# Kernel tuning notes

Measured on AMD Instinct MI355X. Metric: run time of the kernel, lower is better.

## Reference

```python
import jax, jax.numpy as jnp
import numpy as np

N, D, H, L = 50000, 128, 4, 3
E = 800000
C = D // H            # head dim = 32
NEG_SLOPE = 0.2       # PyG GATv2Conv default negative_slope
LN_EPS = 1e-5         # nn.LayerNorm default eps


def setup_inputs() -> dict:
    key = jax.random.key(0)
    ks = jax.random.split(key, 8)
    s = 1.0 / np.sqrt(D).astype(np.float32)
    return {
        "fine_poi_x": jax.random.normal(ks[0], (N, D), jnp.float32),
        "edge_index": jax.random.randint(ks[1], (2, E), 0, N, dtype=jnp.int32),
        "Wl": jax.random.normal(ks[2], (L, D, D), jnp.float32) * s,
        "bl": jnp.zeros((L, D), jnp.float32),
        "Wr": jax.random.normal(ks[3], (L, D, D), jnp.float32) * s,
        "br": jnp.zeros((L, D), jnp.float32),
        "att": jax.random.normal(ks[4], (L, H, C), jnp.float32) * s,
        "bias": jnp.zeros((L, D), jnp.float32),
        "gamma": jnp.ones((L, D), jnp.float32),
        "beta": jnp.zeros((L, D), jnp.float32),
    }


def _gatv2_conv(x, src, dst, Wl, bl, Wr, br, att, bias):
    # x: [N, D]; src/dst: [E'] (self-loops already appended)
    xl = (x @ Wl + bl).reshape(N, H, C)   # source-side transform (lin_l)
    xr = (x @ Wr + br).reshape(N, H, C)   # target-side transform (lin_r)
    m = xl[src] + xr[dst]                 # [E', H, C] per-edge pre-activation
    m = jax.nn.leaky_relu(m, NEG_SLOPE)
    e = jnp.einsum("ehc,hc->eh", m, att)  # [E', H] attention logits
    # segment softmax over edges grouped by destination node
    emax = jax.ops.segment_max(e, dst, num_segments=N)      # [N, H]
    ee = jnp.exp(e - emax[dst])
    denom = jax.ops.segment_sum(ee, dst, num_segments=N)    # [N, H]
    alpha = ee / denom[dst]               # self-loops guarantee denom >= 1 term
    out = jax.ops.segment_sum(xl[src] * alpha[:, :, None], dst, num_segments=N)
    return out.reshape(N, D) + bias


def _layernorm(x, g, b):
    mu = jnp.mean(x, axis=-1, keepdims=True)
    var = jnp.var(x, axis=-1, keepdims=True)
    return (x - mu) * jax.lax.rsqrt(var + LN_EPS) * g + b


def reference(fine_poi_x, edge_index, Wl, bl, Wr, br, att, bias, gamma, beta):
    # PyG GATv2Conv add_self_loops=True: append i->i edges
    loops = jnp.arange(N, dtype=edge_index.dtype)
    src = jnp.concatenate([edge_index[0], loops])
    dst = jnp.concatenate([edge_index[1], loops])
    x = fine_poi_x
    for i in range(L):
        h = _gatv2_conv(x, src, dst, Wl[i], bl[i], Wr[i], br[i], att[i], bias[i])
        x = _layernorm(x + h, gamma[i], beta[i])
        if i != L - 1:
            x = jax.nn.relu(x)
    return x
```

## Files before the change

kernel.cpp:

```cpp
#include <hip/hip_runtime.h>

#define N_NODES 50000
#define N_EDGES 800000
#define DIM 128
#define TOT_EDGES (N_EDGES + N_NODES)
#define LOG2E 1.44269504088896f

#define BSHIFT 9
#define BNODES 512
#define NB ((N_NODES + BNODES - 1) / BNODES)
#define BCAP 16384
#define EPB 4096
#define EPT 16
#define NBLK_A ((TOT_EDGES + EPB - 1) / EPB)

typedef __attribute__((ext_vector_type(8))) _Float16 f16x8;
typedef __attribute__((ext_vector_type(2))) _Float16 h2;
typedef __attribute__((ext_vector_type(4))) float f32x4;
typedef decltype(__builtin_amdgcn_cvt_pkrtz(0.f, 0.f)) fp16v2;

__device__ inline uint h2u(h2 v) { return __builtin_bit_cast(uint, v); }
__device__ inline h2 u2h(uint v) { return __builtin_bit_cast(h2, v); }
__device__ inline uint pk2u(fp16v2 v) { return __builtin_bit_cast(uint, v); }

__device__ inline float rowsum16(float v) {
  int x;
  x = __builtin_amdgcn_update_dpp(0, __float_as_int(v), 0x128, 0xF, 0xF, true);
  v += __int_as_float(x);
  x = __builtin_amdgcn_update_dpp(0, __float_as_int(v), 0x124, 0xF, 0xF, true);
  v += __int_as_float(x);
  x = __builtin_amdgcn_update_dpp(0, __float_as_int(v), 0x122, 0xF, 0xF, true);
  v += __int_as_float(x);
  x = __builtin_amdgcn_update_dpp(0, __float_as_int(v), 0x121, 0xF, 0xF, true);
  v += __int_as_float(x);
  return v;
}

__device__ inline float quadsum4(float v) {
  int x;
  x = __builtin_amdgcn_update_dpp(0, __float_as_int(v), 0xB1, 0xF, 0xF, true);
  v += __int_as_float(x);
  x = __builtin_amdgcn_update_dpp(0, __float_as_int(v), 0x4E, 0xF, 0xF, true);
  v += __int_as_float(x);
  return v;
}


__global__ __launch_bounds__(256) void partA_kernel(const int* __restrict__ srcArr,
                                                    const int* __restrict__ dstArr,
                                                    int* __restrict__ bcnt,
                                                    uint2* __restrict__ bbuf) {
  int tid = threadIdx.x;
  int e0 = blockIdx.x * EPB;
  __shared__ int hist[NB], base[NB], loff[NB];
  if (tid < NB) { hist[tid] = 0; loff[tid] = 0; }
  __syncthreads();

  int sv[EPT], dv[EPT];
#pragma unroll
  for (int i = 0; i < EPT; ++i) {
    int e = e0 + i * 256 + tid;
    int s = 0, d = -1;
    if (e < TOT_EDGES) {
      if (e < N_EDGES) { s = srcArr[e]; d = dstArr[e]; }
      else { s = e - N_EDGES; d = s; }
    }
    sv[i] = s; dv[i] = d;
    if (d >= 0) atomicAdd(&hist[d >> BSHIFT], 1);
  }
  __syncthreads();
  if (tid < NB) {
    int h = hist[tid];
    if (h > 0) base[tid] = atomicAdd(&bcnt[tid], h);
  }
  __syncthreads();
#pragma unroll
  for (int i = 0; i < EPT; ++i) {
    int d = dv[i];
    if (d >= 0) {
      int b = d >> BSHIFT;
      int p = atomicAdd(&loff[b], 1);
      bbuf[(size_t)b * BCAP + base[b] + p] = make_uint2((uint)sv[i], (uint)d);
    }
  }
}

__global__ __launch_bounds__(128) void scanb_kernel(const int* __restrict__ bcnt,
                                                    int* __restrict__ colbase,
                                                    int* __restrict__ rowptr) {
  int tid = threadIdx.x;
  int v = (tid < NB) ? bcnt[tid] : 0;
  __shared__ int s[128];
  s[tid] = v;
  __syncthreads();
  for (int off = 1; off < 128; off <<= 1) {
    int t = (tid >= off) ? s[tid - off] : 0;
    __syncthreads();
    s[tid] += t;
    __syncthreads();
  }
  if (tid < NB) colbase[tid] = s[tid] - v;
  if (tid == 0) rowptr[N_NODES] = TOT_EDGES;
}

__global__ __launch_bounds__(512) void partB_kernel(const uint2* __restrict__ bbuf,
                                                    const int* __restrict__ bcnt,
                                                    const int* __restrict__ colbase,
                                                    int* __restrict__ rowptr,
                                                    int* __restrict__ col) {
  int b = blockIdx.x, tid = threadIdx.x;
  int m = bcnt[b];
  int cb = colbase[b];
  const uint2* buf = bbuf + (size_t)b * BCAP;

  __shared__ int cnt[BNODES], scn[BNODES], cur[BNODES];
  cnt[tid] = 0;
  __syncthreads();
  for (int e = tid; e < m; e += 512) {
    int d = (int)buf[e].y;
    atomicAdd(&cnt[d & (BNODES - 1)], 1);
  }
  __syncthreads();
  int c = cnt[tid];
  scn[tid] = c;
  __syncthreads();
  for (int off = 1; off < BNODES; off <<= 1) {
    int t = (tid >= off) ? scn[tid - off] : 0;
    __syncthreads();
    scn[tid] += t;
    __syncthreads();
  }
  int excl = scn[tid] - c;
  int node = b * BNODES + tid;
  if (node < N_NODES) rowptr[node] = cb + excl;
  cur[tid] = excl;
  __syncthreads();
  for (int e = tid; e < m; e += 512) {
    uint2 sd = buf[e];
    int p = atomicAdd(&cur[(int)sd.y & (BNODES - 1)], 1);
    col[cb + p] = (int)sd.x;
  }
}


__global__ __launch_bounds__(256) void convx_kernel(const float* __restrict__ x,
                                                    uint* __restrict__ xb) {
  int t = blockIdx.x * 256 + threadIdx.x;
  if (t < N_NODES * (DIM / 2)) {
    float2 v = ((const float2*)x)[t];
    xb[t] = pk2u(__builtin_amdgcn_cvt_pkrtz(v.x, v.y));
  }
}

__global__ __launch_bounds__(256) void convw_kernel(const float* __restrict__ Wl,
                                                    const float* __restrict__ Wr,
                                                    ushort* __restrict__ Wt) {
  int t = blockIdx.x * 256 + threadIdx.x;
  if (t >= 3 * 2 * DIM * DIM) return;
  int k = t & 127;
  int n = (t >> 7) & 127;
  int w = (t >> 14) & 1;
  int l = t >> 15;
  const float* W = w ? Wr : Wl;
  _Float16 h = (_Float16)W[l * DIM * DIM + k * DIM + n];
  Wt[t] = __builtin_bit_cast(ushort, h);
}

__global__ __launch_bounds__(192) void conva_kernel(const float* __restrict__ att,
                                                    uint* __restrict__ attc) {
  int t = threadIdx.x;
  float a0 = att[2 * t] * LOG2E, a1 = att[2 * t + 1] * LOG2E;
  attc[t] = pk2u(__builtin_amdgcn_cvt_pkrtz(a0, a1));
}


__global__ __launch_bounds__(256) void gemm_mfma_kernel(
    const uint* __restrict__ xb,
    const ushort* __restrict__ Wt,
    const float* __restrict__ bl, const float* __restrict__ br,
    uint* __restrict__ xl, uint* __restrict__ xr) {
  int wave = threadIdx.x >> 6, lane = threadIdx.x & 63;
  int lr = lane & 15, kq = lane >> 4;
  int m0 = blockIdx.x * 64;

  const ushort* W = Wt + (wave >> 1) * (DIM * DIM);
  const float* bias = (wave >> 1) ? br : bl;
  uint* outp = (wave >> 1) ? xr : xl;
  int n0 = (wave & 1) * 64;

  f16x8 bfrag[4][4];
#pragma unroll
  for (int nt = 0; nt < 4; ++nt)
#pragma unroll
    for (int kt = 0; kt < 4; ++kt)
      bfrag[nt][kt] = *(const f16x8*)(W + (n0 + nt * 16 + lr) * DIM + kt * 32 + kq * 8);

  f32x4 acc[4][4];
#pragma unroll
  for (int mt = 0; mt < 4; ++mt)
#pragma unroll
    for (int nt = 0; nt < 4; ++nt)
      acc[mt][nt] = (f32x4){0.f, 0.f, 0.f, 0.f};

#pragma unroll
  for (int mt = 0; mt < 4; ++mt) {
    int m = m0 + mt * 16 + lr;
    int mc = m < N_NODES ? m : N_NODES - 1;
    f16x8 afrag[4];
#pragma unroll
    for (int kt = 0; kt < 4; ++kt)
      afrag[kt] = *(const f16x8*)((const ushort*)xb + (size_t)mc * DIM + kt * 32 + kq * 8);
#pragma unroll
    for (int nt = 0; nt < 4; ++nt)
#pragma unroll
      for (int kt = 0; kt < 4; ++kt)
        acc[mt][nt] = __builtin_amdgcn_mfma_f32_16x16x32_f16(bfrag[nt][kt], afrag[kt],
                                                             acc[mt][nt], 0, 0, 0);
  }

#pragma unroll
  for (int mt = 0; mt < 4; ++mt) {
    int m = m0 + mt * 16 + lr;
    if (m < N_NODES) {
#pragma unroll
      for (int nt = 0; nt < 4; ++nt) {
        int n = n0 + nt * 16 + kq * 4;
        float4 bb = *(const float4*)(bias + n);
        uint2 o;
        o.x = pk2u(__builtin_amdgcn_cvt_pkrtz(acc[mt][nt][0] + bb.x, acc[mt][nt][1] + bb.y));
        o.y = pk2u(__builtin_amdgcn_cvt_pkrtz(acc[mt][nt][2] + bb.z, acc[mt][nt][3] + bb.w));
        *(uint2*)(outp + (size_t)m * (DIM / 2) + (n >> 1)) = o;
      }
    }
  }
}


__global__ __launch_bounds__(64) void att_kernel(
    const uint4* __restrict__ xinb, const uint4* __restrict__ xlb,
    const uint4* __restrict__ xrb, const int* __restrict__ rowptr,
    const int* __restrict__ col, const uint4* __restrict__ attc,
    const float4* __restrict__ bias, const float4* __restrict__ gamma,
    const float4* __restrict__ beta, uint4* __restrict__ xoutb,
    float4* __restrict__ xoutf, int do_relu) {
  int lane = threadIdx.x;
  int j = lane & 15, e4 = lane >> 4;
  int n = blockIdx.x;

  uint4 rq = xrb[n * 16 + j];
  uint4 aq = attc[j];
  h2 r2[4] = {u2h(rq.x), u2h(rq.y), u2h(rq.z), u2h(rq.w)};
  h2 at2[4] = {u2h(aq.x), u2h(aq.y), u2h(aq.z), u2h(aq.w)};
  const h2 c02 = {(_Float16)0.2f, (_Float16)0.2f};

  h2 accp[4] = {};
  float den = 0.f;

  int js = rowptr[n], je = rowptr[n + 1];
  int jm = je - 1;

  int ci;
  ci = js + e4;      int cA = col[ci < jm ? ci : jm];
  ci = js + 4 + e4;  int cB = col[ci < jm ? ci : jm];
  ci = js + 8 + e4;  int cC = col[ci < jm ? ci : jm];
  uint4 gA = xlb[(size_t)cA * 16 + j];
  uint4 gB = xlb[(size_t)cB * 16 + j];

  for (int cbase = js; cbase < je; cbase += 4) {
    ci = cbase + 12 + e4;
    int cD = col[ci < jm ? ci : jm];
    uint4 gC = xlb[(size_t)cC * 16 + j];

    h2 a0 = u2h(gA.x), a1 = u2h(gA.y), a2 = u2h(gA.z), a3 = u2h(gA.w);
    float p = 0.f;
    {
      h2 s0 = a0 + r2[0], s1 = a1 + r2[1], s2 = a2 + r2[2], s3 = a3 + r2[3];
      h2 m0 = __builtin_elementwise_max(s0, s0 * c02);
      h2 m1 = __builtin_elementwise_max(s1, s1 * c02);
      h2 m2 = __builtin_elementwise_max(s2, s2 * c02);
      h2 m3 = __builtin_elementwise_max(s3, s3 * c02);
      p = __builtin_amdgcn_fdot2(__builtin_bit_cast(fp16v2, m0),
                                 __builtin_bit_cast(fp16v2, at2[0]), p, false);
      p = __builtin_amdgcn_fdot2(__builtin_bit_cast(fp16v2, m1),
                                 __builtin_bit_cast(fp16v2, at2[1]), p, false);
      p = __builtin_amdgcn_fdot2(__builtin_bit_cast(fp16v2, m2),
                                 __builtin_bit_cast(fp16v2, at2[2]), p, false);
      p = __builtin_amdgcn_fdot2(__builtin_bit_cast(fp16v2, m3),
                                 __builtin_bit_cast(fp16v2, at2[3]), p, false);
    }
    p = quadsum4(p);
    float w = (cbase + e4 < je) ? __builtin_amdgcn_exp2f(p) : 0.f;
    den += w;
    _Float16 wh = (_Float16)w;
    h2 w2 = {wh, wh};
    accp[0] = w2 * a0 + accp[0];
    accp[1] = w2 * a1 + accp[1];
    accp[2] = w2 * a2 + accp[2];
    accp[3] = w2 * a3 + accp[3];

    gA = gB; gB = gC; cC = cD;
  }

#pragma unroll
  for (int t = 0; t < 4; ++t) {
    accp[t] += u2h((uint)__shfl_xor((int)h2u(accp[t]), 16, 64));
    accp[t] += u2h((uint)__shfl_xor((int)h2u(accp[t]), 32, 64));
  }
  den += __shfl_xor(den, 16, 64);
  den += __shfl_xor(den, 32, 64);

  float inv = 1.0f / den;
  float acc[8];
#pragma unroll
  for (int t = 0; t < 4; ++t) {
    acc[2 * t] = (float)accp[t].x;
    acc[2 * t + 1] = (float)accp[t].y;
  }

  uint4 xi4 = xinb[n * 16 + j];
  h2 xi[4] = {u2h(xi4.x), u2h(xi4.y), u2h(xi4.z), u2h(xi4.w)};
  float4 b0 = bias[2 * j], b1 = bias[2 * j + 1];

  float o[8];
  o[0] = fmaf(acc[0], inv, b0.x + (float)xi[0].x);
  o[1] = fmaf(acc[1], inv, b0.y + (float)xi[0].y);
  o[2] = fmaf(acc[2], inv, b0.z + (float)xi[1].x);
  o[3] = fmaf(acc[3], inv, b0.w + (float)xi[1].y);
  o[4] = fmaf(acc[4], inv, b1.x + (float)xi[2].x);
  o[5] = fmaf(acc[5], inv, b1.y + (float)xi[2].y);
  o[6] = fmaf(acc[6], inv, b1.z + (float)xi[3].x);
  o[7] = fmaf(acc[7], inv, b1.w + (float)xi[3].y);

  float s1 = 0.f, s2 = 0.f;
#pragma unroll
  for (int t = 0; t < 8; ++t) { s1 += o[t]; s2 = fmaf(o[t], o[t], s2); }
  s1 = rowsum16(s1);
  s2 = rowsum16(s2);
  float mean = s1 * (1.0f / DIM);
  float var = s2 * (1.0f / DIM) - mean * mean;
  float rstd = rsqrtf(var + 1e-5f);

  float4 g0 = gamma[2 * j], g1 = gamma[2 * j + 1];
  float4 t0 = beta[2 * j], t1 = beta[2 * j + 1];
  float y[8];
  y[0] = (o[0] - mean) * rstd * g0.x + t0.x;
  y[1] = (o[1] - mean) * rstd * g0.y + t0.y;
  y[2] = (o[2] - mean) * rstd * g0.z + t0.z;
  y[3] = (o[3] - mean) * rstd * g0.w + t0.w;
  y[4] = (o[4] - mean) * rstd * g1.x + t1.x;
  y[5] = (o[5] - mean) * rstd * g1.y + t1.y;
  y[6] = (o[6] - mean) * rstd * g1.z + t1.z;
  y[7] = (o[7] - mean) * rstd * g1.w + t1.w;
  if (do_relu) {
#pragma unroll
    for (int t = 0; t < 8; ++t) y[t] = fmaxf(y[t], 0.f);
  }

  if (e4 == 0) {
    if (xoutb) {
      uint4 ov;
      ov.x = pk2u(__builtin_amdgcn_cvt_pkrtz(y[0], y[1]));
      ov.y = pk2u(__builtin_amdgcn_cvt_pkrtz(y[2], y[3]));
      ov.z = pk2u(__builtin_amdgcn_cvt_pkrtz(y[4], y[5]));
      ov.w = pk2u(__builtin_amdgcn_cvt_pkrtz(y[6], y[7]));
      xoutb[n * 16 + j] = ov;
    }
    if (xoutf) {
      xoutf[n * 32 + 2 * j] = make_float4(y[0], y[1], y[2], y[3]);
      xoutf[n * 32 + 2 * j + 1] = make_float4(y[4], y[5], y[6], y[7]);
    }
  }
}


extern "C" void kernel_launch(void* const* d_in, const int* in_sizes, int n_in,
                              void* d_out, int out_size, void* d_ws, size_t ws_size,
                              hipStream_t stream) {
  const float* x_in  = (const float*)d_in[0];
  const int*   eidx  = (const int*)d_in[1];
  const float* Wl    = (const float*)d_in[2];
  const float* bl    = (const float*)d_in[3];
  const float* Wr    = (const float*)d_in[4];
  const float* br    = (const float*)d_in[5];
  const float* att   = (const float*)d_in[6];
  const float* bias  = (const float*)d_in[7];
  const float* gamma = (const float*)d_in[8];
  const float* beta  = (const float*)d_in[9];
  float* out = (float*)d_out;

  char* p = (char*)d_ws;
  auto alloc = [&](size_t bytes) {
    char* q = p;
    p += (bytes + 255) & ~(size_t)255;
    return q;
  };
  uint*  xb       = (uint*)alloc((size_t)N_NODES * (DIM / 2) * 4);
  uint*  xlb      = (uint*)alloc((size_t)N_NODES * (DIM / 2) * 4);
  uint*  xrb      = (uint*)alloc((size_t)N_NODES * (DIM / 2) * 4);
  ushort* Wt      = (ushort*)alloc((size_t)3 * 2 * DIM * DIM * 2);
  uint*  attc     = (uint*)alloc((size_t)3 * 64 * 4);
  int*   rowptr   = (int*)alloc((size_t)(N_NODES + 1) * 4);
  int*   col      = (int*)alloc((size_t)TOT_EDGES * 4);
  uint2* bbuf     = (uint2*)alloc((size_t)NB * BCAP * 8);
  int*   bcnt     = (int*)alloc((size_t)NB * 4);
  int*   colbase  = (int*)alloc((size_t)NB * 4);

  (void)hipMemsetAsync(bcnt, 0, (size_t)NB * 4, stream);
  partA_kernel<<<NBLK_A, 256, 0, stream>>>(eidx, eidx + N_EDGES, bcnt, bbuf);
  scanb_kernel<<<1, 128, 0, stream>>>(bcnt, colbase, rowptr);
  partB_kernel<<<NB, 512, 0, stream>>>(bbuf, bcnt, colbase, rowptr, col);
  convx_kernel<<<(N_NODES * (DIM / 2) + 255) / 256, 256, 0, stream>>>(x_in, xb);
  convw_kernel<<<(3 * 2 * DIM * DIM + 255) / 256, 256, 0, stream>>>(Wl, Wr, Wt);
  conva_kernel<<<1, 192, 0, stream>>>(att, attc);

  for (int l = 0; l < 3; ++l) {
    gemm_mfma_kernel<<<(N_NODES + 63) / 64, 256, 0, stream>>>(
        xb, Wt + (size_t)l * 2 * DIM * DIM, bl + l * DIM, br + l * DIM, xlb, xrb);
    att_kernel<<<N_NODES, 64, 0, stream>>>(
        (const uint4*)xb, (const uint4*)xlb, (const uint4*)xrb, rowptr, col,
        (const uint4*)(attc + l * 64), (const float4*)(bias + l * DIM),
        (const float4*)(gamma + l * DIM), (const float4*)(beta + l * DIM),
        (l == 2) ? nullptr : (uint4*)xb, (l == 2) ? (float4*)out : nullptr,
        (l != 2) ? 1 : 0);
  }
}
```

Before: 248.8 us.

## Make attention kernel persistent with grid-stride waves and deeper gather prefetch

```diff
diff --git a/kernel.cpp b/kernel.cpp
--- a/kernel.cpp
+++ b/kernel.cpp
@@ -13,6 +13,9 @@
 #define EPB 4096
 #define EPT 16
 #define NBLK_A ((TOT_EDGES + EPB - 1) / EPB)
+
+#define ATT_BLOCKS 2048
+#define ATT_WAVES (ATT_BLOCKS * 4)
 
 typedef __attribute__((ext_vector_type(8))) _Float16 f16x8;
 typedef __attribute__((ext_vector_type(2))) _Float16 h2;
@@ -236,138 +239,143 @@
 }
 
 
-__global__ __launch_bounds__(64) void att_kernel(
+__global__ __launch_bounds__(256) void att_kernel(
     const uint4* __restrict__ xinb, const uint4* __restrict__ xlb,
     const uint4* __restrict__ xrb, const int* __restrict__ rowptr,
     const int* __restrict__ col, const uint4* __restrict__ attc,
     const float4* __restrict__ bias, const float4* __restrict__ gamma,
     const float4* __restrict__ beta, uint4* __restrict__ xoutb,
     float4* __restrict__ xoutf, int do_relu) {
-  int lane = threadIdx.x;
+  int lane = threadIdx.x & 63;
+  int wid = blockIdx.x * 4 + (threadIdx.x >> 6);
   int j = lane & 15, e4 = lane >> 4;
-  int n = blockIdx.x;
-
-  uint4 rq = xrb[n * 16 + j];
+
   uint4 aq = attc[j];
-  h2 r2[4] = {u2h(rq.x), u2h(rq.y), u2h(rq.z), u2h(rq.w)};
   h2 at2[4] = {u2h(aq.x), u2h(aq.y), u2h(aq.z), u2h(aq.w)};
   const h2 c02 = {(_Float16)0.2f, (_Float16)0.2f};
-
-  h2 accp[4] = {};
-  float den = 0.f;
-
-  int js = rowptr[n], je = rowptr[n + 1];
-  int jm = je - 1;
-
-  int ci;
-  ci = js + e4;      int cA = col[ci < jm ? ci : jm];
-  ci = js + 4 + e4;  int cB = col[ci < jm ? ci : jm];
-  ci = js + 8 + e4;  int cC = col[ci < jm ? ci : jm];
-  uint4 gA = xlb[(size_t)cA * 16 + j];
-  uint4 gB = xlb[(size_t)cB * 16 + j];
-
-  for (int cbase = js; cbase < je; cbase += 4) {
-    ci = cbase + 12 + e4;
-    int cD = col[ci < jm ? ci : jm];
+  float4 b0 = bias[2 * j], b1 = bias[2 * j + 1];
+  float4 gm0 = gamma[2 * j], gm1 = gamma[2 * j + 1];
+  float4 bt0 = beta[2 * j], bt1 = beta[2 * j + 1];
+
+  for (int n = wid; n < N_NODES; n += ATT_WAVES) {
+    uint4 rq = xrb[n * 16 + j];
+    h2 r2[4] = {u2h(rq.x), u2h(rq.y), u2h(rq.z), u2h(rq.w)};
+
+    h2 accp[4] = {};
+    float den = 0.f;
+
+    int js = rowptr[n], je = rowptr[n + 1];
+    int jm = je - 1;
+
+    int ci;
+    ci = js + e4;       int cA = col[ci < jm ? ci : jm];
+    ci = js + 4 + e4;   int cB = col[ci < jm ? ci : jm];
+    ci = js + 8 + e4;   int cC = col[ci < jm ? ci : jm];
+    ci = js + 12 + e4;  int cD = col[ci < jm ? ci : jm];
+    uint4 gA = xlb[(size_t)cA * 16 + j];
+    uint4 gB = xlb[(size_t)cB * 16 + j];
     uint4 gC = xlb[(size_t)cC * 16 + j];
 
-    h2 a0 = u2h(gA.x), a1 = u2h(gA.y), a2 = u2h(gA.z), a3 = u2h(gA.w);
-    float p = 0.f;
-    {
-      h2 s0 = a0 + r2[0], s1 = a1 + r2[1], s2 = a2 + r2[2], s3 = a3 + r2[3];
-      h2 m0 = __builtin_elementwise_max(s0, s0 * c02);
-      h2 m1 = __builtin_elementwise_max(s1, s1 * c02);
-      h2 m2 = __builtin_elementwise_max(s2, s2 * c02);
-      h2 m3 = __builtin_elementwise_max(s3, s3 * c02);
-      p = __builtin_amdgcn_fdot2(__builtin_bit_cast(fp16v2, m0),
-                                 __builtin_bit_cast(fp16v2, at2[0]), p, false);
-      p = __builtin_amdgcn_fdot2(__builtin_bit_cast(fp16v2, m1),
-                                 __builtin_bit_cast(fp16v2, at2[1]), p, false);
-      p = __builtin_amdgcn_fdot2(__builtin_bit_cast(fp16v2, m2),
-                                 __builtin_bit_cast(fp16v2, at2[2]), p, false);
-      p = __builtin_amdgcn_fdot2(__builtin_bit_cast(fp16v2, m3),
-                                 __builtin_bit_cast(fp16v2, at2[3]), p, false);
-    }
-    p = quadsum4(p);
-    float w = (cbase + e4 < je) ? __builtin_amdgcn_exp2f(p) : 0.f;
-    den += w;
-    _Float16 wh = (_Float16)w;
-    h2 w2 = {wh, wh};
-    accp[0] = w2 * a0 + accp[0];
-    accp[1] = w2 * a1 + accp[1];
-    accp[2] = w2 * a2 + accp[2];
-    accp[3] = w2 * a3 + accp[3];
-
-    gA = gB; gB = gC; cC = cD;
-  }
-
-#pragma unroll
-  for (int t = 0; t < 4; ++t) {
-    accp[t] += u2h((uint)__shfl_xor((int)h2u(accp[t]), 16, 64));
-    accp[t] += u2h((uint)__shfl_xor((int)h2u(accp[t]), 32, 64));
-  }
-  den += __shfl_xor(den, 16, 64);
-  den += __shfl_xor(den, 32, 64);
-
-  float inv = 1.0f / den;
-  float acc[8];
-#pragma unroll
-  for (int t = 0; t < 4; ++t) {
-    acc[2 * t] = (float)accp[t].x;
-    acc[2 * t + 1] = (float)accp[t].y;
-  }
-
-  uint4 xi4 = xinb[n * 16 + j];
-  h2 xi[4] = {u2h(xi4.x), u2h(xi4.y), u2h(xi4.z), u2h(xi4.w)};
-  float4 b0 = bias[2 * j], b1 = bias[2 * j + 1];
-
-  float o[8];
-  o[0] = fmaf(acc[0], inv, b0.x + (float)xi[0].x);
-  o[1] = fmaf(acc[1], inv, b0.y + (float)xi[0].y);
-  o[2] = fmaf(acc[2], inv, b0.z + (float)xi[1].x);
-  o[3] = fmaf(acc[3], inv, b0.w + (float)xi[1].y);
-  o[4] = fmaf(acc[4], inv, b1.x + (float)xi[2].x);
-  o[5] = fmaf(acc[5], inv, b1.y + (float)xi[2].y);
-  o[6] = fmaf(acc[6], inv, b1.z + (float)xi[3].x);
-  o[7] = fmaf(acc[7], inv, b1.w + (float)xi[3].y);
-
-  float s1 = 0.f, s2 = 0.f;
-#pragma unroll
-  for (int t = 0; t < 8; ++t) { s1 += o[t]; s2 = fmaf(o[t], o[t], s2); }
-  s1 = rowsum16(s1);
-  s2 = rowsum16(s2);
-  float mean = s1 * (1.0f / DIM);
-  float var = s2 * (1.0f / DIM) - mean * mean;
-  float rstd = rsqrtf(var + 1e-5f);
-
-  float4 g0 = gamma[2 * j], g1 = gamma[2 * j + 1];
-  float4 t0 = beta[2 * j], t1 = beta[2 * j + 1];
-  float y[8];
-  y[0] = (o[0] - mean) * rstd * g0.x + t0.x;
-  y[1] = (o[1] - mean) * rstd * g0.y + t0.y;
-  y[2] = (o[2] - mean) * rstd * g0.z + t0.z;
-  y[3] = (o[3] - mean) * rstd * g0.w + t0.w;
-  y[4] = (o[4] - mean) * rstd * g1.x + t1.x;
-  y[5] = (o[5] - mean) * rstd * g1.y + t1.y;
-  y[6] = (o[6] - mean) * rstd * g1.z + t1.z;
-  y[7] = (o[7] - mean) * rstd * g1.w + t1.w;
-  if (do_relu) {
-#pragma unroll
-    for (int t = 0; t < 8; ++t) y[t] = fmaxf(y[t], 0.f);
-  }
-
-  if (e4 == 0) {
-    if (xoutb) {
-      uint4 ov;
-      ov.x = pk2u(__builtin_amdgcn_cvt_pkrtz(y[0], y[1]));
-      ov.y = pk2u(__builtin_amdgcn_cvt_pkrtz(y[2], y[3]));
-      ov.z = pk2u(__builtin_amdgcn_cvt_pkrtz(y[4], y[5]));
-      ov.w = pk2u(__builtin_amdgcn_cvt_pkrtz(y[6], y[7]));
-      xoutb[n * 16 + j] = ov;
-    }
-    if (xoutf) {
-      xoutf[n * 32 + 2 * j] = make_float4(y[0], y[1], y[2], y[3]);
-      xoutf[n * 32 + 2 * j + 1] = make_float4(y[4], y[5], y[6], y[7]);
+    for (int cbase = js; cbase < je; cbase += 4) {
+      ci = cbase + 16 + e4;
+      int cE = col[ci < jm ? ci : jm];
+      uint4 gD = xlb[(size_t)cD * 16 + j];
+
+      h2 a0 = u2h(gA.x), a1 = u2h(gA.y), a2 = u2h(gA.z), a3 = u2h(gA.w);
+      float p = 0.f;
+      {
+        h2 s0 = a0 + r2[0], s1 = a1 + r2[1], s2 = a2 + r2[2], s3 = a3 + r2[3];
+        h2 m0 = __builtin_elementwise_max(s0, s0 * c02);
+        h2 m1 = __builtin_elementwise_max(s1, s1 * c02);
+        h2 m2 = __builtin_elementwise_max(s2, s2 * c02);
+        h2 m3 = __builtin_elementwise_max(s3, s3 * c02);
+        p = __builtin_amdgcn_fdot2(__builtin_bit_cast(fp16v2, m0),
+                                   __builtin_bit_cast(fp16v2, at2[0]), p, false);
+        p = __builtin_amdgcn_fdot2(__builtin_bit_cast(fp16v2, m1),
+                                   __builtin_bit_cast(fp16v2, at2[1]), p, false);
+        p = __builtin_amdgcn_fdot2(__builtin_bit_cast(fp16v2, m2),
+                                   __builtin_bit_cast(fp16v2, at2[2]), p, false);
+        p = __builtin_amdgcn_fdot2(__builtin_bit_cast(fp16v2, m3),
+                                   __builtin_bit_cast(fp16v2, at2[3]), p, false);
+      }
+      p = quadsum4(p);
+      float w = (cbase + e4 < je) ? __builtin_amdgcn_exp2f(p) : 0.f;
+      den += w;
+      _Float16 wh = (_Float16)w;
+      h2 w2 = {wh, wh};
+      accp[0] = w2 * a0 + accp[0];
+      accp[1] = w2 * a1 + accp[1];
+      accp[2] = w2 * a2 + accp[2];
+      accp[3] = w2 * a3 + accp[3];
+
+      gA = gB; gB = gC; gC = gD; cD = cE;
+    }
+
+#pragma unroll
+    for (int t = 0; t < 4; ++t) {
+      accp[t] += u2h((uint)__shfl_xor((int)h2u(accp[t]), 16, 64));
+      accp[t] += u2h((uint)__shfl_xor((int)h2u(accp[t]), 32, 64));
+    }
+    den += __shfl_xor(den, 16, 64);
+    den += __shfl_xor(den, 32, 64);
+
+    float inv = 1.0f / den;
+    float acc[8];
+#pragma unroll
+    for (int t = 0; t < 4; ++t) {
+      acc[2 * t] = (float)accp[t].x;
+      acc[2 * t + 1] = (float)accp[t].y;
+    }
+
+    uint4 xi4 = xinb[n * 16 + j];
+    h2 xi[4] = {u2h(xi4.x), u2h(xi4.y), u2h(xi4.z), u2h(xi4.w)};
+
+    float o[8];
+    o[0] = fmaf(acc[0], inv, b0.x + (float)xi[0].x);
+    o[1] = fmaf(acc[1], inv, b0.y + (float)xi[0].y);
+    o[2] = fmaf(acc[2], inv, b0.z + (float)xi[1].x);
+    o[3] = fmaf(acc[3], inv, b0.w + (float)xi[1].y);
+    o[4] = fmaf(acc[4], inv, b1.x + (float)xi[2].x);
+    o[5] = fmaf(acc[5], inv, b1.y + (float)xi[2].y);
+    o[6] = fmaf(acc[6], inv, b1.z + (float)xi[3].x);
+    o[7] = fmaf(acc[7], inv, b1.w + (float)xi[3].y);
+
+    float s1 = 0.f, s2 = 0.f;
+#pragma unroll
+    for (int t = 0; t < 8; ++t) { s1 += o[t]; s2 = fmaf(o[t], o[t], s2); }
+    s1 = rowsum16(s1);
+    s2 = rowsum16(s2);
+    float mean = s1 * (1.0f / DIM);
+    float var = s2 * (1.0f / DIM) - mean * mean;
+    float rstd = rsqrtf(var + 1e-5f);
+
+    float y[8];
+    y[0] = (o[0] - mean) * rstd * gm0.x + bt0.x;
+    y[1] = (o[1] - mean) * rstd * gm0.y + bt0.y;
+    y[2] = (o[2] - mean) * rstd * gm0.z + bt0.z;
+    y[3] = (o[3] - mean) * rstd * gm0.w + bt0.w;
+    y[4] = (o[4] - mean) * rstd * gm1.x + bt1.x;
+    y[5] = (o[5] - mean) * rstd * gm1.y + bt1.y;
+    y[6] = (o[6] - mean) * rstd * gm1.z + bt1.z;
+    y[7] = (o[7] - mean) * rstd * gm1.w + bt1.w;
+    if (do_relu) {
+#pragma unroll
+      for (int t = 0; t < 8; ++t) y[t] = fmaxf(y[t], 0.f);
+    }
+
+    if (e4 == 0) {
+      if (xoutb) {
+        uint4 ov;
+        ov.x = pk2u(__builtin_amdgcn_cvt_pkrtz(y[0], y[1]));
+        ov.y = pk2u(__builtin_amdgcn_cvt_pkrtz(y[2], y[3]));
+        ov.z = pk2u(__builtin_amdgcn_cvt_pkrtz(y[4], y[5]));
+        ov.w = pk2u(__builtin_amdgcn_cvt_pkrtz(y[6], y[7]));
+        xoutb[n * 16 + j] = ov;
+      }
+      if (xoutf) {
+        xoutf[n * 32 + 2 * j] = make_float4(y[0], y[1], y[2], y[3]);
+        xoutf[n * 32 + 2 * j + 1] = make_float4(y[4], y[5], y[6], y[7]);
+      }
     }
   }
 }
@@ -416,7 +424,7 @@
   for (int l = 0; l < 3; ++l) {
     gemm_mfma_kernel<<<(N_NODES + 63) / 64, 256, 0, stream>>>(
         xb, Wt + (size_t)l * 2 * DIM * DIM, bl + l * DIM, br + l * DIM, xlb, xrb);
-    att_kernel<<<N_NODES, 64, 0, stream>>>(
+    att_kernel<<<ATT_BLOCKS, 256, 0, stream>>>(
         (const uint4*)xb, (const uint4*)xlb, (const uint4*)xrb, rowptr, col,
         (const uint4*)(attc + l * 64), (const float4*)(bias + l * DIM),
         (const float4*)(gamma + l * DIM), (const float4*)(beta + l * DIM),
```

Result: slower. 305.1 us (+22.6%).
